# Kernel tuning notes

Hardware: AMD Instinct MI355X
Metric: run time of the kernel (lower is better)

Reference implementation:

```python
import jax, jax.numpy as jnp
import numpy as np

N, K, C = 2, 512, 256
IMG = 1024.0
P = 7            # output_size
S = 2            # sampling_ratio
SCALES = (0.25, 0.125, 0.0625, 0.03125)
MIN_LEVEL, MAX_LEVEL = 2, 5
CANON_SIZE, CANON_LEVEL = 224.0, 4


def setup_inputs() -> dict:
    key = jax.random.key(0)
    ks = jax.random.split(key, 7)
    feats = {}
    for i, (hw, kk) in enumerate(zip((256, 128, 64, 32), ks[:4])):
        feats[f"feat{i + 2}"] = jax.random.normal(kk, (N, C, hw, hw), dtype=jnp.float32)
    # boxes: centers uniform in image, sizes log-uniform in [32, 512] px -> spans all levels
    cxy = jax.random.uniform(ks[4], (N, K, 2), minval=0.0, maxval=IMG)
    wh = 32.0 * jnp.exp2(jax.random.uniform(ks[5], (N, K, 2), minval=0.0, maxval=4.0))
    x1y1 = jnp.clip(cxy - wh / 2, 0.0, IMG)
    x2y2 = jnp.clip(cxy + wh / 2, 0.0, IMG)
    boxes = jnp.concatenate([x1y1, x2y2], axis=-1).astype(jnp.float32)  # [N,K,4] xyxy
    feats["boxes"] = boxes
    return feats


def _roi_align_level(feat, boxes, batch_idx, scale):
    """ROIAlignV2 (aligned=True). feat [N,C,H,W], boxes [M,4] xyxy in image coords."""
    Nf, Cf, H, W = feat.shape
    M = boxes.shape[0]
    b = boxes * scale - 0.5  # aligned=True shift
    x1, y1, x2, y2 = b[:, 0], b[:, 1], b[:, 2], b[:, 3]
    bin_h = (y2 - y1) / P
    bin_w = (x2 - x1) / P
    # combined bin+sample grid: coord = start + ((i + 0.5)/S) * bin, i in [0, P*S)
    g = (jnp.arange(P * S, dtype=feat.dtype) + 0.5) / S  # [PS]
    y = y1[:, None] + g[None, :] * bin_h[:, None]  # [M, PS]
    x = x1[:, None] + g[None, :] * bin_w[:, None]  # [M, PS]

    def prep(c, size):
        valid = (c >= -1.0) & (c <= size)
        c = jnp.maximum(c, 0.0)
        lo = jnp.minimum(jnp.floor(c).astype(jnp.int32), size - 1)
        hi = jnp.minimum(lo + 1, size - 1)
        frac = c - lo.astype(c.dtype)  # harmless if >1 when lo==hi==size-1
        return lo, hi, frac, valid

    yl, yh, fy, vy = prep(y, H)
    xl, xh, fx, vx = prep(x, W)
    bi = batch_idx[:, None, None]

    def gather(yy, xx):
        # -> [M, PS, PS, C]
        return feat[bi, :, yy[:, :, None], xx[:, None, :]]

    fy_ = fy[:, :, None, None]
    fx_ = fx[:, None, :, None]
    v = ((1 - fy_) * ((1 - fx_) * gather(yl, xl) + fx_ * gather(yl, xh))
         + fy_ * ((1 - fx_) * gather(yh, xl) + fx_ * gather(yh, xh)))
    mask = (vy[:, :, None] & vx[:, None, :])[..., None]
    v = jnp.where(mask, v, jnp.zeros((), feat.dtype))
    out = v.reshape(M, P, S, P, S, Cf).mean(axis=(2, 4))  # avg over sampling grid
    return out.transpose(0, 3, 1, 2)  # [M, C, P, P]


def reference(feat2, feat3, feat4, feat5, boxes):
    feats = [feat2, feat3, feat4, feat5]
    flat = boxes.reshape(-1, 4)  # [M,4], concat over images
    batch_idx = jnp.repeat(jnp.arange(N, dtype=jnp.int32), K)
    # assign_boxes_to_levels
    area = (flat[:, 2] - flat[:, 0]) * (flat[:, 3] - flat[:, 1])
    sizes = jnp.sqrt(area)
    lvl = jnp.floor(CANON_LEVEL + jnp.log2(sizes / CANON_SIZE + 1e-8))
    lvl = jnp.clip(lvl, MIN_LEVEL, MAX_LEVEL).astype(jnp.int32) - MIN_LEVEL  # [M] in 0..3
    out = jnp.zeros((flat.shape[0], C, P, P), dtype=feat2.dtype)
    for l, (feat, scale) in enumerate(zip(feats, SCALES)):
        o = _roi_align_level(feat, flat, batch_idx, scale)
        out = jnp.where((lvl == l)[:, None, None, None], o, out)
    return out
```

## Files before the change

kernel.cpp:

```cpp
#include <hip/hip_runtime.h>
#include <math.h>
#include <stdint.h>

#define NBATCH 2
#define KBOX   512
#define NBOX   (NBATCH*KBOX)
#define CCH    256
#define NBIN   49
#define NCH    4
#define BPB    (CCH/NCH)
#define COUT   (CCH*NBIN)
#define WCAP   1152
#define HDRN   8
#define TAPN   (24*NBIN)

typedef const uint32_t __attribute__((address_space(1)))* gas_u32p;
typedef uint32_t       __attribute__((address_space(3)))* las_u32p;

__global__ __launch_bounds__(64) void box_prep_kernel(
    const float* __restrict__ boxes, int* __restrict__ hdr, int* __restrict__ taps)
{
    const int m    = blockIdx.x;
    const int lane = threadIdx.x;

    const float x1 = boxes[m*4+0];
    const float y1 = boxes[m*4+1];
    const float x2 = boxes[m*4+2];
    const float y2 = boxes[m*4+3];

    const float area = (x2 - x1) * (y2 - y1);
    const float size = sqrtf(area);
    float lvlf = floorf(4.0f + log2f(size / 224.0f + 1e-8f));
    lvlf = fminf(fmaxf(lvlf, 2.0f), 5.0f);
    const int lvl = (int)lvlf - 2;

    const int   H     = 256 >> lvl;
    const float scale = 0.25f / (float)(1 << lvl);
    const float Hf    = (float)H;

    const float bx1 = x1 * scale - 0.5f;
    const float by1 = y1 * scale - 0.5f;
    const float bin_w = (x2 * scale - 0.5f - bx1) / 7.0f;
    const float bin_h = (y2 * scale - 0.5f - by1) / 7.0f;

    const float sx_min = bx1 + 0.25f * bin_w;
    const float sx_max = bx1 + 6.75f * bin_w;
    const float sy_min = by1 + 0.25f * bin_h;
    const float sy_max = by1 + 6.75f * bin_h;
    const int wx0 = min((int)floorf(fmaxf(sx_min, 0.0f)), H - 1);
    const int wy0 = min((int)floorf(fmaxf(sy_min, 0.0f)), H - 1);
    const int wx1 = min(min((int)floorf(fmaxf(sx_max, 0.0f)), H - 1) + 1, H - 1);
    const int wy1 = min(min((int)floorf(fmaxf(sy_max, 0.0f)), H - 1) + 1, H - 1);
    const int wspan = wx1 - wx0 + 1;
    const int hspan = wy1 - wy0 + 1;
    const int wsz   = wspan * hspan;

    if (lane < NBIN) {
        const int py = lane / 7;
        const int px = lane - py * 7;
        const int base = m * TAPN;
        float* tapf = (float*)taps;

        #pragma unroll
        for (int s = 0; s < 4; ++s) {
            const int iy = s >> 1;
            const int ix = s & 1;
            const float gy = ((float)(2*py + iy) + 0.5f) * 0.5f;
            const float gx = ((float)(2*px + ix) + 0.5f) * 0.5f;
            const float yy = by1 + gy * bin_h;
            const float xx = bx1 + gx * bin_w;

            const bool valid = (yy >= -1.0f) && (yy <= Hf) && (xx >= -1.0f) && (xx <= Hf);

            const float yc = fmaxf(yy, 0.0f);
            const float xc = fmaxf(xx, 0.0f);
            int yl = min((int)floorf(yc), H - 1);
            int xl = min((int)floorf(xc), H - 1);
            const int yh = min(yl + 1, H - 1);
            const int xh = min(xl + 1, H - 1);
            const float fy = yc - (float)yl;
            float fx = xc - (float)xl;
            if (xh == xl) fx = 0.0f;

            const float vm  = valid ? 0.25f : 0.0f;
            const float wyl = (1.0f - fy) * vm;
            const float wyh = fy * vm;

            const int xr = xl - wx0;
            const int o_lo = (yl - wy0) * wspan + xr;
            const int o_hi = (yh - wy0) * wspan + xr;

            taps[base + (2*s  )*NBIN + lane] = o_lo;
            taps[base + (2*s+1)*NBIN + lane] = o_hi;
            tapf[base + (8 + 2*s  )*NBIN + lane] = wyl * (1.0f - fx);
            tapf[base + (8 + 2*s+1)*NBIN + lane] = wyh * (1.0f - fx);
            tapf[base + (16 + 2*s  )*NBIN + lane] = wyl * fx;
            tapf[base + (16 + 2*s+1)*NBIN + lane] = wyh * fx;
        }
    }

    if (lane == 0) {
        int* h = hdr + m * HDRN;
        h[0] = lvl;
        h[1] = H;
        h[2] = H * H;
        h[3] = wy0 * H + wx0;
        h[4] = wspan;
        h[5] = wsz;
        h[6] = __float_as_int(1.0f / (float)wspan);
    }
}

__global__ __launch_bounds__(256, 8) void roi_align_kernel(
    const float* __restrict__ f2, const float* __restrict__ f3,
    const float* __restrict__ f4, const float* __restrict__ f5,
    const int* __restrict__ hdr, const int* __restrict__ taps,
    float* __restrict__ out)
{
    const int bid  = blockIdx.x;
    const int m    = bid >> 6;
    const int cg   = bid & 63;
    const int tid  = threadIdx.x;
    const int lane = tid & 63;
    const int wid  = tid >> 6;
    const int b    = m >> 9;

    __shared__ float win[NCH * WCAP];

    const int* h = hdr + m * HDRN;
    const int   lvl   = h[0];
    const int   H     = h[1];
    const int   HH    = h[2];
    const int   woff  = h[3];
    const int   wspan = h[4];
    const int   wsz   = h[5];
    const float rw    = __int_as_float(h[6]);

    const float* fptr = (lvl == 0) ? f2 : (lvl == 1) ? f3 : (lvl == 2) ? f4 : f5;
    const int c = cg * NCH + wid;
    const float* src0 = fptr + ((size_t)(b * CCH + c)) * HH + woff;
    float* wbase = win + wid * WCAP;

    for (int i = lane; i < wsz; i += 64) {
        const int r   = (int)(((float)i + 0.5f) * rw);
        const int col = i - r * wspan;
        __builtin_amdgcn_global_load_lds(
            (gas_u32p)(const void*)(src0 + r * H + col),
            (las_u32p)(void*)(&wbase[i & ~63]),
            4, 0, 0);
    }
    if (lane == 0) wbase[wsz] = 0.0f;

    const int lidx = (lane < NBIN) ? lane : NBIN - 1;
    const int tb = m * TAPN;
    const float* tf = (const float*)taps;

    int   o8 [8];
    float wlo[8];
    float whi[8];
    #pragma unroll
    for (int j = 0; j < 8; ++j) o8 [j] = taps[tb + j*NBIN + lidx];
    #pragma unroll
    for (int j = 0; j < 8; ++j) wlo[j] = tf[tb + (8  + j)*NBIN + lidx];
    #pragma unroll
    for (int j = 0; j < 8; ++j) whi[j] = tf[tb + (16 + j)*NBIN + lidx];

    asm volatile("s_waitcnt vmcnt(0) lgkmcnt(0)" ::: "memory");
    __builtin_amdgcn_sched_barrier(0);

    float acc = 0.0f;
    #pragma unroll
    for (int j = 0; j < 8; ++j) {
        const int oj = o8[j];
        acc += wlo[j] * wbase[oj] + whi[j] * wbase[oj + 1];
    }

    if (lane < NBIN) {
        __builtin_nontemporal_store(
            acc, out + (size_t)m * COUT + (size_t)c * NBIN + lane);
    }
}

extern "C" void kernel_launch(void* const* d_in, const int* in_sizes, int n_in,
                              void* d_out, int out_size, void* d_ws, size_t ws_size,
                              hipStream_t stream) {
    const float* f2    = (const float*)d_in[0];
    const float* f3    = (const float*)d_in[1];
    const float* f4    = (const float*)d_in[2];
    const float* f5    = (const float*)d_in[3];
    const float* boxes = (const float*)d_in[4];
    float* outp = (float*)d_out;

    int* hdr  = (int*)d_ws;
    int* taps = (int*)d_ws + NBOX * HDRN;

    box_prep_kernel<<<dim3(NBOX), dim3(64), 0, stream>>>(boxes, hdr, taps);
    roi_align_kernel<<<dim3(NBOX * BPB), dim3(256), 0, stream>>>(
        f2, f3, f4, f5, hdr, taps, outp);
}
```

Baseline: 117.4 us.

## Use 16-byte LDS window loads, pack taps in fp16, reorder block-to-box mapping

The feature-window staging now uses 16-byte global_load_lds transfers over a 4-float-aligned window instead of per-element 4-byte loads. Tap offsets are packed as two 16-bit values and bilinear weights are stored as half2, halving tap table traffic. The block index is remapped so that 8 consecutive blocks cover different boxes, and occupancy hints drop to 5 blocks to fit the larger LDS window. The fp16 weights lose some precision, and the aligned window loads extra columns.

```diff
diff --git a/kernel.cpp b/kernel.cpp
--- a/kernel.cpp
+++ b/kernel.cpp
@@ -1,4 +1,5 @@
 #include <hip/hip_runtime.h>
+#include <hip/hip_fp16.h>
 #include <math.h>
 #include <stdint.h>
 
@@ -10,15 +11,15 @@
 #define NCH    4
 #define BPB    (CCH/NCH)
 #define COUT   (CCH*NBIN)
-#define WCAP   1152
+#define WCAP   1800
 #define HDRN   8
-#define TAPN   (24*NBIN)
+#define TAPN   (12*NBIN)
 
 typedef const uint32_t __attribute__((address_space(1)))* gas_u32p;
 typedef uint32_t       __attribute__((address_space(3)))* las_u32p;
 
 __global__ __launch_bounds__(64) void box_prep_kernel(
-    const float* __restrict__ boxes, int* __restrict__ hdr, int* __restrict__ taps)
+    const float* __restrict__ boxes, int* __restrict__ hdr, uint32_t* __restrict__ taps)
 {
     const int m    = blockIdx.x;
     const int lane = threadIdx.x;
@@ -51,15 +52,18 @@
     const int wy0 = min((int)floorf(fmaxf(sy_min, 0.0f)), H - 1);
     const int wx1 = min(min((int)floorf(fmaxf(sx_max, 0.0f)), H - 1) + 1, H - 1);
     const int wy1 = min(min((int)floorf(fmaxf(sy_max, 0.0f)), H - 1) + 1, H - 1);
-    const int wspan = wx1 - wx0 + 1;
     const int hspan = wy1 - wy0 + 1;
-    const int wsz   = wspan * hspan;
+
+    const int wx0a = wx0 & ~3;
+    const int wsp4 = ((wx1 - wx0a + 4) >> 2) << 2;
+    const int qpr  = wsp4 >> 2;
+    const int nq   = hspan * qpr;
 
     if (lane < NBIN) {
         const int py = lane / 7;
         const int px = lane - py * 7;
-        const int base = m * TAPN;
-        float* tapf = (float*)taps;
+        const uint32_t base = (uint32_t)m * TAPN;
+        __half2* th = (__half2*)taps;
 
         #pragma unroll
         for (int s = 0; s < 4; ++s) {
@@ -86,16 +90,13 @@
             const float wyl = (1.0f - fy) * vm;
             const float wyh = fy * vm;
 
-            const int xr = xl - wx0;
-            const int o_lo = (yl - wy0) * wspan + xr;
-            const int o_hi = (yh - wy0) * wspan + xr;
-
-            taps[base + (2*s  )*NBIN + lane] = o_lo;
-            taps[base + (2*s+1)*NBIN + lane] = o_hi;
-            tapf[base + (8 + 2*s  )*NBIN + lane] = wyl * (1.0f - fx);
-            tapf[base + (8 + 2*s+1)*NBIN + lane] = wyh * (1.0f - fx);
-            tapf[base + (16 + 2*s  )*NBIN + lane] = wyl * fx;
-            tapf[base + (16 + 2*s+1)*NBIN + lane] = wyh * fx;
+            const int xr  = xl - wx0a;
+            const uint32_t olo = (uint32_t)((yl - wy0) * wsp4 + xr);
+            const uint32_t ohi = (uint32_t)((yh - wy0) * wsp4 + xr);
+
+            taps[base + s*NBIN + lane] = olo | (ohi << 16);
+            th  [base + (4+s)*NBIN + lane] = __floats2half2_rn(wyl*(1.0f-fx), wyh*(1.0f-fx));
+            th  [base + (8+s)*NBIN + lane] = __floats2half2_rn(wyl*fx,        wyh*fx);
         }
     }
 
@@ -104,22 +105,23 @@
         h[0] = lvl;
         h[1] = H;
         h[2] = H * H;
-        h[3] = wy0 * H + wx0;
-        h[4] = wspan;
-        h[5] = wsz;
-        h[6] = __float_as_int(1.0f / (float)wspan);
+        h[3] = wy0 * H + wx0a;
+        h[4] = qpr;
+        h[5] = nq;
+        h[6] = __float_as_int(1.0f / (float)qpr);
+        h[7] = nq << 2;
     }
 }
 
-__global__ __launch_bounds__(256, 8) void roi_align_kernel(
+__global__ __launch_bounds__(256, 5) void roi_align_kernel(
     const float* __restrict__ f2, const float* __restrict__ f3,
     const float* __restrict__ f4, const float* __restrict__ f5,
-    const int* __restrict__ hdr, const int* __restrict__ taps,
+    const int* __restrict__ hdr, const uint32_t* __restrict__ taps,
     float* __restrict__ out)
 {
     const int bid  = blockIdx.x;
-    const int m    = bid >> 6;
-    const int cg   = bid & 63;
+    const int cg   = (bid >> 3) & 63;
+    const int m    = (bid & 7) | ((bid >> 9) << 3);
     const int tid  = threadIdx.x;
     const int lane = tid & 63;
     const int wid  = tid >> 6;
@@ -128,51 +130,55 @@
     __shared__ float win[NCH * WCAP];
 
     const int* h = hdr + m * HDRN;
-    const int   lvl   = h[0];
-    const int   H     = h[1];
-    const int   HH    = h[2];
-    const int   woff  = h[3];
-    const int   wspan = h[4];
-    const int   wsz   = h[5];
-    const float rw    = __int_as_float(h[6]);
+    const int   lvl  = h[0];
+    const int   H    = h[1];
+    const int   HH   = h[2];
+    const int   woff = h[3];
+    const int   qpr  = h[4];
+    const int   nq   = h[5];
+    const float rq   = __int_as_float(h[6]);
+    const int   nq4  = h[7];
 
     const float* fptr = (lvl == 0) ? f2 : (lvl == 1) ? f3 : (lvl == 2) ? f4 : f5;
     const int c = cg * NCH + wid;
     const float* src0 = fptr + ((size_t)(b * CCH + c)) * HH + woff;
     float* wbase = win + wid * WCAP;
 
-    for (int i = lane; i < wsz; i += 64) {
-        const int r   = (int)(((float)i + 0.5f) * rw);
-        const int col = i - r * wspan;
+    for (int iq = lane; iq < nq; iq += 64) {
+        const int r  = (int)(((float)iq + 0.5f) * rq);
+        const int c4 = (iq - r * qpr) << 2;
         __builtin_amdgcn_global_load_lds(
-            (gas_u32p)(const void*)(src0 + r * H + col),
-            (las_u32p)(void*)(&wbase[i & ~63]),
-            4, 0, 0);
-    }
-    if (lane == 0) wbase[wsz] = 0.0f;
-
-    const int lidx = (lane < NBIN) ? lane : NBIN - 1;
-    const int tb = m * TAPN;
-    const float* tf = (const float*)taps;
-
-    int   o8 [8];
-    float wlo[8];
-    float whi[8];
-    #pragma unroll
-    for (int j = 0; j < 8; ++j) o8 [j] = taps[tb + j*NBIN + lidx];
-    #pragma unroll
-    for (int j = 0; j < 8; ++j) wlo[j] = tf[tb + (8  + j)*NBIN + lidx];
-    #pragma unroll
-    for (int j = 0; j < 8; ++j) whi[j] = tf[tb + (16 + j)*NBIN + lidx];
+            (gas_u32p)(const void*)(src0 + r * H + c4),
+            (las_u32p)(void*)(&wbase[(iq & ~63) << 2]),
+            16, 0, 0);
+    }
+    if (lane == 0) wbase[nq4] = 0.0f;
+
+    const int l = (lane < NBIN) ? lane : NBIN - 1;
+    const uint32_t* tb = taps + (uint32_t)m * TAPN;
+    const __half2*  th = (const __half2*)tb;
+
+    uint32_t po[4];
+    __half2  wl[4], wh[4];
+    #pragma unroll
+    for (int s = 0; s < 4; ++s) po[s] = tb[s*NBIN + l];
+    #pragma unroll
+    for (int s = 0; s < 4; ++s) wl[s] = th[(4+s)*NBIN + l];
+    #pragma unroll
+    for (int s = 0; s < 4; ++s) wh[s] = th[(8+s)*NBIN + l];
 
     asm volatile("s_waitcnt vmcnt(0) lgkmcnt(0)" ::: "memory");
     __builtin_amdgcn_sched_barrier(0);
 
     float acc = 0.0f;
     #pragma unroll
-    for (int j = 0; j < 8; ++j) {
-        const int oj = o8[j];
-        acc += wlo[j] * wbase[oj] + whi[j] * wbase[oj + 1];
+    for (int s = 0; s < 4; ++s) {
+        const int olo = (int)(po[s] & 0xffffu);
+        const int ohi = (int)(po[s] >> 16);
+        const float2 a  = __half22float2(wl[s]);
+        const float2 bw = __half22float2(wh[s]);
+        acc += a.x * wbase[olo] + bw.x * wbase[olo + 1];
+        acc += a.y * wbase[ohi] + bw.y * wbase[ohi + 1];
     }
 
     if (lane < NBIN) {
@@ -191,8 +197,8 @@
     const float* boxes = (const float*)d_in[4];
     float* outp = (float*)d_out;
 
-    int* hdr  = (int*)d_ws;
-    int* taps = (int*)d_ws + NBOX * HDRN;
+    int*      hdr  = (int*)d_ws;
+    uint32_t* taps = (uint32_t*)d_ws + NBOX * HDRN;
 
     box_prep_kernel<<<dim3(NBOX), dim3(64), 0, stream>>>(boxes, hdr, taps);
     roi_align_kernel<<<dim3(NBOX * BPB), dim3(256), 0, stream>>>(
```

Result: slower. 163.1 us (+39.0%).
